# Optimization experiments

Measured on AMD Instinct MI355X. Metric: run time of the kernel, lower is better.

The kernel has to match this reference:

```python
import jax, jax.numpy as jnp
import numpy as np

N_NODES = 100000
N_REL = 8
F_IN, F_HID, F_OUT = 64, 64, 32
N_EDGES = 1000000


def rgcn_conv(x, W, root, bias, src, dst, edge_type):
    """PyG RGCNConv with default aggr='mean': out[i] = sum_r mean_{j in N_r(i)} W_r x_j + root x_i + bias."""
    R, _, O = W.shape
    N = x.shape[0]
    # Transform every node under every relation: [R, N, O]
    h = jnp.einsum('nf,rfo->rno', x, W)
    # Gather per-edge messages: [E, O]
    msg = h[edge_type, src]
    # Per-(relation, dst) mean aggregation via combined segment ids
    seg = edge_type * N + dst
    sums = jax.ops.segment_sum(msg, seg, num_segments=R * N).reshape(R, N, O)
    cnt = jax.ops.segment_sum(jnp.ones((msg.shape[0],), msg.dtype), seg,
                              num_segments=R * N).reshape(R, N, 1)
    mean = sums / jnp.maximum(cnt, 1.0)  # empty neighborhoods -> 0
    return mean.sum(axis=0) + x @ root + bias


def setup_inputs() -> dict:
    key = jax.random.key(0)
    ks = jax.random.split(key, 9)
    s = lambda fan: 1.0 / np.sqrt(fan)
    x = jax.random.normal(ks[0], (N_NODES, F_IN), jnp.float32)
    edge_index = jax.random.randint(ks[1], (2, N_EDGES), 0, N_NODES, jnp.int64)
    edge_type = jax.random.randint(ks[2], (N_EDGES,), 0, N_REL, jnp.int64)
    W1 = jax.random.normal(ks[3], (N_REL, F_IN, F_HID), jnp.float32) * s(F_IN)
    root1 = jax.random.normal(ks[4], (F_IN, F_HID), jnp.float32) * s(F_IN)
    b1 = jnp.zeros((F_HID,), jnp.float32)
    W2 = jax.random.normal(ks[5], (N_REL, F_HID, F_OUT), jnp.float32) * s(F_HID)
    root2 = jax.random.normal(ks[6], (F_HID, F_OUT), jnp.float32) * s(F_HID)
    b2 = jnp.zeros((F_OUT,), jnp.float32)
    return {"x": x, "W1": W1, "root1": root1, "b1": b1,
            "W2": W2, "root2": root2, "b2": b2,
            "edge_index": edge_index, "edge_type": edge_type}


def reference(x, W1, root1, b1, W2, root2, b2, edge_index, edge_type):
    src, dst = edge_index[0], edge_index[1]
    # encode (dropout is identity in eval mode)
    h = jax.nn.relu(rgcn_conv(x, W1, root1, b1, src, dst, edge_type))
    z = rgcn_conv(h, W2, root2, b2, src, dst, edge_type)
    # decode: gather-dot-product link scores over the same edge list
    return (z[src] * z[dst]).sum(axis=1)
```

## Files before the change

### kernel.cpp

```cpp
#include <hip/hip_runtime.h>

#define F_IN 64
#define F_HID 64
#define F_OUT 32
#define NREL 8
#define SCAP 6144
#define RCAP 10240
#define MAXBUCK 200
#define PA_PE 16

typedef __attribute__((ext_vector_type(8))) short bfrag;
typedef __attribute__((ext_vector_type(4))) float ffrag;

__device__ inline unsigned short f2bf(float f) {
  unsigned u = __float_as_uint(f);
  unsigned r = (u + 0x7fffu + ((u >> 16) & 1u)) >> 16;
  return (unsigned short)r;
}
__device__ inline unsigned bf16pair(float lo, float hi) {
  return (unsigned)f2bf(lo) | ((unsigned)f2bf(hi) << 16);
}
__device__ inline float bflo(unsigned u) { return __uint_as_float(u << 16); }
__device__ inline float bfhi(unsigned u) { return __uint_as_float(u & 0xffff0000u); }

__device__ inline void acc8(float (&acc)[8], float s, uint4 g) {
  acc[0] += s * bflo(g.x); acc[1] += s * bfhi(g.x);
  acc[2] += s * bflo(g.y); acc[3] += s * bfhi(g.y);
  acc[4] += s * bflo(g.z); acc[5] += s * bfhi(g.z);
  acc[6] += s * bflo(g.w); acc[7] += s * bfhi(g.w);
}
__device__ inline float dot8(uint4 a, uint4 b) {
  return bflo(a.x) * bflo(b.x) + bfhi(a.x) * bfhi(b.x) +
         bflo(a.y) * bflo(b.y) + bfhi(a.y) * bfhi(b.y) +
         bflo(a.z) * bflo(b.z) + bfhi(a.z) * bfhi(b.z) +
         bflo(a.w) * bflo(b.w) + bfhi(a.w) * bfhi(b.w);
}

template <int O, bool PERMK>
__device__ inline void wprep_one(int t, const float* __restrict__ W,
                                 const float* __restrict__ root,
                                 unsigned short* __restrict__ Wf) {
  constexpr int CT = O / 16;
  int l = t & 63;
  int s = (t >> 6) & 1;
  int rc = t >> 7;
  int c = rc % CT;
  int r = rc / CT;
  const float* wsrc = (r < NREL) ? W + (size_t)r * 64 * O : root;
  unsigned short* dst = Wf + (size_t)t * 8;
  int col = c * 16 + (l & 15);
  int k0 = s * 32 + ((l >> 4) * 8);
#pragma unroll
  for (int j = 0; j < 8; ++j) {
    int k = k0 + j;
    if (PERMK) k = (k & 3) * 16 + (k >> 2);
    dst[j] = f2bf(wsrc[(size_t)k * O + col]);
  }
}

__global__ __launch_bounds__(256) void prep_kernel(
    const float* __restrict__ W1, const float* __restrict__ root1,
    const float* __restrict__ W2, const float* __restrict__ root2,
    unsigned short* __restrict__ wf1, unsigned short* __restrict__ wf2,
    int* __restrict__ gcur, int nbuck) {
  int gid = blockIdx.x * 256 + threadIdx.x;
  const int J1 = (NREL + 1) * (F_HID / 16) * 2 * 64;
  const int J2 = (NREL + 1) * (F_OUT / 16) * 2 * 64;
  if (gid < J1) {
    wprep_one<F_HID, false>(gid, W1, root1, wf1);
  } else if (gid < J1 + J2) {
    wprep_one<F_OUT, true>(gid - J1, W2, root2, wf2);
  } else if (gid - J1 - J2 < nbuck) {
    int b = gid - J1 - J2;
    gcur[b] = b * SCAP;
  }
}

__device__ void binA_body(
    const int* __restrict__ src, const int* __restrict__ dst,
    const int* __restrict__ et, int* __restrict__ gcur,
    unsigned* __restrict__ staging, int E) {
  __shared__ int hist[MAXBUCK * 4];
  __shared__ int wbase[MAXBUCK * 4];
  const int tid = threadIdx.x;
  const int wave = tid >> 6;
  for (int i = tid; i < MAXBUCK * 4; i += 256) hist[i] = 0;
  __syncthreads();
  const int base = blockIdx.x * (256 * PA_PE);
  int dv[PA_PE], rk[PA_PE];
#pragma unroll
  for (int j = 0; j < PA_PE; ++j) {
    int e = base + j * 256 + tid;
    if (e < E) {
      int d = dst[e];
      dv[j] = d;
      rk[j] = atomicAdd(&hist[(d >> 9) * 4 + wave], 1);
    } else {
      dv[j] = -1;
    }
  }
  __syncthreads();
  for (int b = tid; b < MAXBUCK; b += 256) {
    int h0 = hist[b * 4 + 0], h1 = hist[b * 4 + 1];
    int h2 = hist[b * 4 + 2], h3 = hist[b * 4 + 3];
    int tot = h0 + h1 + h2 + h3;
    int gb = tot ? atomicAdd(&gcur[b], tot) : 0;
    wbase[b * 4 + 0] = gb;
    wbase[b * 4 + 1] = gb + h0;
    wbase[b * 4 + 2] = gb + h0 + h1;
    wbase[b * 4 + 3] = gb + h0 + h1 + h2;
  }
  __syncthreads();
#pragma unroll
  for (int j = 0; j < PA_PE; ++j) {
    if (dv[j] >= 0) {
      int e = base + j * 256 + tid;
      unsigned pk = (unsigned)src[e] | ((unsigned)et[e] << 17) |
                    ((unsigned)(dv[j] & 511) << 20);
      staging[wbase[(dv[j] >> 9) * 4 + wave] + rk[j]] = pk;
    }
  }
}

__global__ __launch_bounds__(256) void binB_kernel(
    const unsigned* __restrict__ staging, const int* __restrict__ gcur,
    int2* __restrict__ rec, int* __restrict__ startsA, int* __restrict__ endsA,
    int N) {
  __shared__ int cnt8[512 * 8];
  __shared__ int cur[512];
  __shared__ int tsum[256];
  const int b = blockIdx.x;
  const int tid = threadIdx.x;
  const int n0 = b << 9;
  const int nn = min(512, N - n0);
  const int cnt_b = gcur[b] - b * SCAP;
  const unsigned* st = staging + (size_t)b * SCAP;
  for (int i = tid; i < 512 * 8; i += 256) cnt8[i] = 0;
  __syncthreads();
  for (int i = tid; i < cnt_b; i += 256) {
    unsigned e = st[i];
    atomicAdd(&cnt8[((e >> 20) & 511) * 8 + ((e >> 17) & 7)], 1);
  }
  __syncthreads();
  const int na = 2 * tid, nb = 2 * tid + 1;
  int deg0 = 0, deg1 = 0;
#pragma unroll
  for (int r = 0; r < 8; ++r) {
    deg0 += cnt8[na * 8 + r];
    deg1 += cnt8[nb * 8 + r];
  }
  const int pd0 = (deg0 + 7) & ~7, pd1 = (deg1 + 7) & ~7;
  tsum[tid] = pd0 + pd1;
  __syncthreads();
  for (int off = 1; off < 256; off <<= 1) {
    int v = (tid >= off) ? tsum[tid - off] : 0;
    __syncthreads();
    tsum[tid] += v;
    __syncthreads();
  }
  const int excl = tsum[tid] - (pd0 + pd1);
  const int s0 = b * RCAP + excl;
  const int s1 = s0 + pd0;
  if (na < nn) { startsA[n0 + na] = s0; endsA[n0 + na] = s0 + pd0; cur[na] = s0; }
  if (nb < nn) { startsA[n0 + nb] = s1; endsA[n0 + nb] = s1 + pd1; cur[nb] = s1; }
  __syncthreads();
  for (int i = tid; i < 512 * 8; i += 256) {
    int cc = cnt8[i];
    ((float*)cnt8)[i] = cc > 0 ? 1.0f / (float)cc : 0.0f;
  }
  __syncthreads();
  for (int i = tid; i < cnt_b; i += 256) {
    unsigned e = st[i];
    int s = e & 0x1FFFF;
    int r = (e >> 17) & 7;
    int dl = (e >> 20) & 511;
    int pos = atomicAdd(&cur[dl], 1);
    rec[pos] = make_int2(r * N + s, ((const int*)cnt8)[dl * 8 + r]);
  }
  __syncthreads();
  if (na < nn) for (int p = cur[na]; p < s0 + pd0; ++p) rec[p] = make_int2(0, 0);
  if (nb < nn) for (int p = cur[nb]; p < s1 + pd1; ++p) rec[p] = make_int2(0, 0);
}

template <int O, bool F32IN>
__device__ void transform_body(int blk, const void* __restrict__ Xv,
                               const unsigned short* __restrict__ Wf,
                               unsigned short* __restrict__ H, int N) {
  constexpr int CT = O / 16;
  const int w = threadIdx.x >> 6;
  const int l = threadIdx.x & 63;
  const int nb = blk * 64;
  int arow = nb + w * 16 + (l & 15);
  if (arow >= N) arow = N - 1;
  bfrag a0, a1;
  if (F32IN) {
    const float* xf = (const float*)Xv + (size_t)arow * 64 + ((l >> 4) * 8);
    float4 v0 = *(const float4*)(xf);
    float4 v1 = *(const float4*)(xf + 4);
    float4 v2 = *(const float4*)(xf + 32);
    float4 v3 = *(const float4*)(xf + 36);
    a0[0] = (short)f2bf(v0.x); a0[1] = (short)f2bf(v0.y);
    a0[2] = (short)f2bf(v0.z); a0[3] = (short)f2bf(v0.w);
    a0[4] = (short)f2bf(v1.x); a0[5] = (short)f2bf(v1.y);
    a0[6] = (short)f2bf(v1.z); a0[7] = (short)f2bf(v1.w);
    a1[0] = (short)f2bf(v2.x); a1[1] = (short)f2bf(v2.y);
    a1[2] = (short)f2bf(v2.z); a1[3] = (short)f2bf(v2.w);
    a1[4] = (short)f2bf(v3.x); a1[5] = (short)f2bf(v3.y);
    a1[6] = (short)f2bf(v3.z); a1[7] = (short)f2bf(v3.w);
  } else {
    const unsigned short* xp = (const unsigned short*)Xv + (size_t)arow * 64 + ((l >> 4) * 8);
    a0 = *(const bfrag*)(xp);
    a1 = *(const bfrag*)(xp + 32);
  }
  const int rbase = nb + w * 16 + ((l >> 4) << 2);
  for (int r = 0; r < NREL + 1; ++r) {
    const unsigned short* wb = Wf + ((size_t)r * CT * 2 * 64 + l) * 8;
    ffrag acc[CT];
#pragma unroll
    for (int c = 0; c < CT; ++c) {
      bfrag b0 = *(const bfrag*)(wb + (size_t)(c * 2 + 0) * 512);
      bfrag b1 = *(const bfrag*)(wb + (size_t)(c * 2 + 1) * 512);
      ffrag z = {0.f, 0.f, 0.f, 0.f};
      acc[c] = __builtin_amdgcn_mfma_f32_16x16x32_bf16(a0, b0, z, 0, 0, 0);
      acc[c] = __builtin_amdgcn_mfma_f32_16x16x32_bf16(a1, b1, acc[c], 0, 0, 0);
    }
#pragma unroll
    for (int i = 0; i < 4; ++i) {
      int row = rbase + i;
      if (row < N) {
        if (O == 64) {
          uint2 v;
          v.x = bf16pair(acc[0][i], acc[1][i]);
          v.y = bf16pair(acc[2][i], acc[3][i]);
          *(uint2*)(H + ((size_t)r * N + row) * 64 + (l & 15) * 4) = v;
        } else {
          *(unsigned*)(H + ((size_t)r * N + row) * 32 + (l & 15) * 2) =
              bf16pair(acc[0][i], acc[1][i]);
        }
      }
    }
  }
}

__global__ __launch_bounds__(256) void binA_t1_kernel(
    const int* __restrict__ src, const int* __restrict__ dst,
    const int* __restrict__ et, int* __restrict__ gcur,
    unsigned* __restrict__ staging, int E, int nbinA,
    const float* __restrict__ x, const unsigned short* __restrict__ wf1,
    unsigned short* __restrict__ h, int N) {
  if ((int)blockIdx.x < nbinA) {
    binA_body(src, dst, et, gcur, staging, E);
  } else {
    transform_body<F_HID, true>((int)blockIdx.x - nbinA, x, wf1, h, N);
  }
}

__global__ __launch_bounds__(256) void transform2_kernel(
    const unsigned short* __restrict__ Xb, const unsigned short* __restrict__ Wf,
    unsigned short* __restrict__ H, int N) {
  transform_body<F_OUT, false>((int)blockIdx.x, Xb, Wf, H, N);
}

template <int O, bool RELU>
__global__ __launch_bounds__(256) void csr_agg_kernel(
    const unsigned* __restrict__ H, const int* __restrict__ startsA,
    const int* __restrict__ endsA, const int2* __restrict__ rec,
    const float* __restrict__ bias, unsigned* __restrict__ Y, int N) {
  constexpr int C = O / 8;
  constexpr int NPB = 256 / C;
  constexpr int HROW = O / 2;
  constexpr int CT = O / 16;
  int t = threadIdx.x;
  int n = blockIdx.x * NPB + t / C;
  int c = t % C;
  if (n >= N) return;
  float acc[8];
  uint4 rr = *(const uint4*)(H + ((size_t)(NREL * N) + n) * HROW + c * 4);
#pragma unroll
  for (int j = 0; j < 8; ++j) {
    int q = c * 8 + j;
    acc[j] = bias[(q % CT) * 16 + q / CT];
  }
  acc[0] += bflo(rr.x); acc[1] += bfhi(rr.x);
  acc[2] += bflo(rr.y); acc[3] += bfhi(rr.y);
  acc[4] += bflo(rr.z); acc[5] += bfhi(rr.z);
  acc[6] += bflo(rr.w); acc[7] += bfhi(rr.w);
  int p = startsA[n];
  int end = endsA[n];
  for (; p < end; p += 8) {
    int4 e01 = *(const int4*)(rec + p);
    int4 e23 = *(const int4*)(rec + p + 2);
    int4 e45 = *(const int4*)(rec + p + 4);
    int4 e67 = *(const int4*)(rec + p + 6);
    uint4 g0 = *(const uint4*)(H + (size_t)e01.x * HROW + c * 4);
    uint4 g1 = *(const uint4*)(H + (size_t)e01.z * HROW + c * 4);
    uint4 g2 = *(const uint4*)(H + (size_t)e23.x * HROW + c * 4);
    uint4 g3 = *(const uint4*)(H + (size_t)e23.z * HROW + c * 4);
    uint4 g4 = *(const uint4*)(H + (size_t)e45.x * HROW + c * 4);
    uint4 g5 = *(const uint4*)(H + (size_t)e45.z * HROW + c * 4);
    uint4 g6 = *(const uint4*)(H + (size_t)e67.x * HROW + c * 4);
    uint4 g7 = *(const uint4*)(H + (size_t)e67.z * HROW + c * 4);
    acc8(acc, __int_as_float(e01.y), g0);
    acc8(acc, __int_as_float(e01.w), g1);
    acc8(acc, __int_as_float(e23.y), g2);
    acc8(acc, __int_as_float(e23.w), g3);
    acc8(acc, __int_as_float(e45.y), g4);
    acc8(acc, __int_as_float(e45.w), g5);
    acc8(acc, __int_as_float(e67.y), g6);
    acc8(acc, __int_as_float(e67.w), g7);
  }
  if (RELU) {
#pragma unroll
    for (int j = 0; j < 8; ++j) acc[j] = fmaxf(acc[j], 0.f);
  }
  uint4 o;
  o.x = bf16pair(acc[0], acc[1]);
  o.y = bf16pair(acc[2], acc[3]);
  o.z = bf16pair(acc[4], acc[5]);
  o.w = bf16pair(acc[6], acc[7]);
  *(uint4*)(Y + (size_t)n * HROW + c * 4) = o;
}

__global__ __launch_bounds__(256) void decode_kernel(
    const unsigned* __restrict__ Z, const int* __restrict__ src,
    const int* __restrict__ dst, float* __restrict__ out, int E) {
  int e = blockIdx.x * blockDim.x + threadIdx.x;
  if (e >= E) return;
  const uint4* zs = (const uint4*)(Z + (size_t)src[e] * 16);
  const uint4* zd = (const uint4*)(Z + (size_t)dst[e] * 16);
  uint4 a0 = zs[0], a1 = zs[1], a2 = zs[2], a3 = zs[3];
  uint4 b0 = zd[0], b1 = zd[1], b2 = zd[2], b3 = zd[3];
  out[e] = dot8(a0, b0) + dot8(a1, b1) + dot8(a2, b2) + dot8(a3, b3);
}

extern "C" void kernel_launch(void* const* d_in, const int* in_sizes, int n_in,
                              void* d_out, int out_size, void* d_ws, size_t ws_size,
                              hipStream_t stream) {
  const float* x     = (const float*)d_in[0];
  const float* W1    = (const float*)d_in[1];
  const float* root1 = (const float*)d_in[2];
  const float* b1    = (const float*)d_in[3];
  const float* W2    = (const float*)d_in[4];
  const float* root2 = (const float*)d_in[5];
  const float* b2    = (const float*)d_in[6];
  const int*   ei    = (const int*)d_in[7];
  const int*   et    = (const int*)d_in[8];

  const int N = in_sizes[0] / F_IN;
  const int E = in_sizes[8];
  const int nbuck = (N + 511) >> 9;
  const int nbinA = (E + 256 * PA_PE - 1) / (256 * PA_PE);
  const int nT1 = (N + 63) / 64;
  const int* srcp = ei;
  const int* dstp = ei + E;

  char* ws = (char*)d_ws;
  int*            gcur    = (int*)(ws + 0);
  unsigned*       staging = (unsigned*)(ws + 4096);
  int*            startsA = (int*)(ws + 4919296);
  int*            endsA   = (int*)(ws + 5319296);
  int2*           rec     = (int2*)(ws + 5719296);
  unsigned short* wf1     = (unsigned short*)(ws + 21775616);
  unsigned short* wf2     = (unsigned short*)(ws + 21849344);
  unsigned short* h       = (unsigned short*)(ws + 21886208);
  unsigned short* hmid    = (unsigned short*)(ws + 137086208);
  unsigned short* z       = (unsigned short*)(ws + 149886208);

  prep_kernel<<<28, 256, 0, stream>>>(W1, root1, W2, root2, wf1, wf2, gcur, nbuck);

  binA_t1_kernel<<<nbinA + nT1, 256, 0, stream>>>(
      srcp, dstp, et, gcur, staging, E, nbinA, x, wf1, h, N);

  binB_kernel<<<nbuck, 256, 0, stream>>>(staging, gcur, rec, startsA, endsA, N);

  csr_agg_kernel<F_HID, true>
      <<<(N + 31) / 32, 256, 0, stream>>>((const unsigned*)h, startsA, endsA, rec,
                                          b1, (unsigned*)hmid, N);

  transform2_kernel<<<(N + 63) / 64, 256, 0, stream>>>(hmid, wf2, h, N);
  csr_agg_kernel<F_OUT, false>
      <<<(N + 63) / 64, 256, 0, stream>>>((const unsigned*)h, startsA, endsA, rec,
                                          b2, (unsigned*)z, N);

  decode_kernel<<<(E + 255) / 256, 256, 0, stream>>>((const unsigned*)z, srcp, dstp,
                                                     (float*)d_out, E);
}
```

Before: 161.2 us.

## Split transform and aggregation stages to co-schedule them with bin and aggregate kernels

Splits the first-layer transform so part of it runs alongside binA and the rest fills the small binB launch. Splits the first aggregation in two, so the second half runs in the same launch as the second-layer transform over rows the first half has already finished. Adds a separate h2 buffer so the second transform does not overwrite h1 while it is still being read. The aim is to fill idle compute units during under-occupied stages. In exchange it adds one more launch, uses more workspace, and relies on fixed split sizes (600 and 1800 blocks).

```diff
diff --git a/kernel.cpp b/kernel.cpp
--- a/kernel.cpp
+++ b/kernel.cpp
@@ -122,14 +122,13 @@
   }
 }
 
-__global__ __launch_bounds__(256) void binB_kernel(
-    const unsigned* __restrict__ staging, const int* __restrict__ gcur,
+__device__ void binB_body(
+    int b, const unsigned* __restrict__ staging, const int* __restrict__ gcur,
     int2* __restrict__ rec, int* __restrict__ startsA, int* __restrict__ endsA,
     int N) {
   __shared__ int cnt8[512 * 8];
   __shared__ int cur[512];
   __shared__ int tsum[256];
-  const int b = blockIdx.x;
   const int tid = threadIdx.x;
   const int n0 = b << 9;
   const int nn = min(512, N - n0);
@@ -242,28 +241,9 @@
   }
 }
 
-__global__ __launch_bounds__(256) void binA_t1_kernel(
-    const int* __restrict__ src, const int* __restrict__ dst,
-    const int* __restrict__ et, int* __restrict__ gcur,
-    unsigned* __restrict__ staging, int E, int nbinA,
-    const float* __restrict__ x, const unsigned short* __restrict__ wf1,
-    unsigned short* __restrict__ h, int N) {
-  if ((int)blockIdx.x < nbinA) {
-    binA_body(src, dst, et, gcur, staging, E);
-  } else {
-    transform_body<F_HID, true>((int)blockIdx.x - nbinA, x, wf1, h, N);
-  }
-}
-
-__global__ __launch_bounds__(256) void transform2_kernel(
-    const unsigned short* __restrict__ Xb, const unsigned short* __restrict__ Wf,
-    unsigned short* __restrict__ H, int N) {
-  transform_body<F_OUT, false>((int)blockIdx.x, Xb, Wf, H, N);
-}
-
 template <int O, bool RELU>
-__global__ __launch_bounds__(256) void csr_agg_kernel(
-    const unsigned* __restrict__ H, const int* __restrict__ startsA,
+__device__ void csr_agg_body(
+    int blk, const unsigned* __restrict__ H, const int* __restrict__ startsA,
     const int* __restrict__ endsA, const int2* __restrict__ rec,
     const float* __restrict__ bias, unsigned* __restrict__ Y, int N) {
   constexpr int C = O / 8;
@@ -271,7 +251,7 @@
   constexpr int HROW = O / 2;
   constexpr int CT = O / 16;
   int t = threadIdx.x;
-  int n = blockIdx.x * NPB + t / C;
+  int n = blk * NPB + t / C;
   int c = t % C;
   if (n >= N) return;
   float acc[8];
@@ -321,6 +301,67 @@
   *(uint4*)(Y + (size_t)n * HROW + c * 4) = o;
 }
 
+__global__ __launch_bounds__(256) void binA_t1a_kernel(
+    const int* __restrict__ src, const int* __restrict__ dst,
+    const int* __restrict__ et, int* __restrict__ gcur,
+    unsigned* __restrict__ staging, int E, int nbinA,
+    const float* __restrict__ x, const unsigned short* __restrict__ wf1,
+    unsigned short* __restrict__ h1, int N) {
+  if ((int)blockIdx.x < nbinA) {
+    binA_body(src, dst, et, gcur, staging, E);
+  } else {
+    transform_body<F_HID, true>((int)blockIdx.x - nbinA, x, wf1, h1, N);
+  }
+}
+
+__global__ __launch_bounds__(256) void binB_t1b_kernel(
+    const unsigned* __restrict__ staging, const int* __restrict__ gcur,
+    int2* __restrict__ rec, int* __restrict__ startsA, int* __restrict__ endsA,
+    int nbuck, int nT1a, const float* __restrict__ x,
+    const unsigned short* __restrict__ wf1, unsigned short* __restrict__ h1,
+    int N) {
+  if ((int)blockIdx.x < nbuck) {
+    binB_body((int)blockIdx.x, staging, gcur, rec, startsA, endsA, N);
+  } else {
+    transform_body<F_HID, true>(nT1a + (int)blockIdx.x - nbuck, x, wf1, h1, N);
+  }
+}
+
+__global__ __launch_bounds__(256) void agg1a_kernel(
+    const unsigned* __restrict__ H, const int* __restrict__ startsA,
+    const int* __restrict__ endsA, const int2* __restrict__ rec,
+    const float* __restrict__ bias, unsigned* __restrict__ Y, int N) {
+  csr_agg_body<F_HID, true>((int)blockIdx.x, H, startsA, endsA, rec, bias, Y, N);
+}
+
+__global__ __launch_bounds__(256) void agg1b_t2a_kernel(
+    const unsigned* __restrict__ H1, const int* __restrict__ startsA,
+    const int* __restrict__ endsA, const int2* __restrict__ rec,
+    const float* __restrict__ b1, unsigned* __restrict__ hmid,
+    int nAgg1a, int nAgg1b, const unsigned short* __restrict__ wf2,
+    unsigned short* __restrict__ h2, int N) {
+  if ((int)blockIdx.x < nAgg1b) {
+    csr_agg_body<F_HID, true>(nAgg1a + (int)blockIdx.x, H1, startsA, endsA, rec,
+                              b1, hmid, N);
+  } else {
+    transform_body<F_OUT, false>((int)blockIdx.x - nAgg1b,
+                                 (const unsigned short*)hmid, wf2, h2, N);
+  }
+}
+
+__global__ __launch_bounds__(256) void t2b_kernel(
+    const unsigned short* __restrict__ hmid, const unsigned short* __restrict__ wf2,
+    unsigned short* __restrict__ h2, int nT2a, int N) {
+  transform_body<F_OUT, false>(nT2a + (int)blockIdx.x, hmid, wf2, h2, N);
+}
+
+__global__ __launch_bounds__(256) void agg2_kernel(
+    const unsigned* __restrict__ H2, const int* __restrict__ startsA,
+    const int* __restrict__ endsA, const int2* __restrict__ rec,
+    const float* __restrict__ bias, unsigned* __restrict__ Y, int N) {
+  csr_agg_body<F_OUT, false>((int)blockIdx.x, H2, startsA, endsA, rec, bias, Y, N);
+}
+
 __global__ __launch_bounds__(256) void decode_kernel(
     const unsigned* __restrict__ Z, const int* __restrict__ src,
     const int* __restrict__ dst, float* __restrict__ out, int E) {
@@ -351,6 +392,15 @@
   const int nbuck = (N + 511) >> 9;
   const int nbinA = (E + 256 * PA_PE - 1) / (256 * PA_PE);
   const int nT1 = (N + 63) / 64;
+  const int nT1a = nT1 < 600 ? nT1 : 600;
+  const int nT1b = nT1 - nT1a;
+  const int nAgg1 = (N + 31) / 32;
+  const int nAgg1a = nAgg1 < 1800 ? nAgg1 : 1800;
+  const int nAgg1b = nAgg1 - nAgg1a;
+  const int nT2 = (N + 63) / 64;
+  int nT2a = (nAgg1a * 32) / 64;
+  if (nT2a > nT2) nT2a = nT2;
+  const int nT2b = nT2 - nT2a;
   const int* srcp = ei;
   const int* dstp = ei + E;
 
@@ -362,25 +412,30 @@
   int2*           rec     = (int2*)(ws + 5719296);
   unsigned short* wf1     = (unsigned short*)(ws + 21775616);
   unsigned short* wf2     = (unsigned short*)(ws + 21849344);
-  unsigned short* h       = (unsigned short*)(ws + 21886208);
+  unsigned short* h1      = (unsigned short*)(ws + 21886208);
   unsigned short* hmid    = (unsigned short*)(ws + 137086208);
   unsigned short* z       = (unsigned short*)(ws + 149886208);
+  unsigned short* h2      = (unsigned short*)(ws + 156286208);
 
   prep_kernel<<<28, 256, 0, stream>>>(W1, root1, W2, root2, wf1, wf2, gcur, nbuck);
 
-  binA_t1_kernel<<<nbinA + nT1, 256, 0, stream>>>(
-      srcp, dstp, et, gcur, staging, E, nbinA, x, wf1, h, N);
-
-  binB_kernel<<<nbuck, 256, 0, stream>>>(staging, gcur, rec, startsA, endsA, N);
-
-  csr_agg_kernel<F_HID, true>
-      <<<(N + 31) / 32, 256, 0, stream>>>((const unsigned*)h, startsA, endsA, rec,
-                                          b1, (unsigned*)hmid, N);
-
-  transform2_kernel<<<(N + 63) / 64, 256, 0, stream>>>(hmid, wf2, h, N);
-  csr_agg_kernel<F_OUT, false>
-      <<<(N + 63) / 64, 256, 0, stream>>>((const unsigned*)h, startsA, endsA, rec,
-                                          b2, (unsigned*)z, N);
+  binA_t1a_kernel<<<nbinA + nT1a, 256, 0, stream>>>(
+      srcp, dstp, et, gcur, staging, E, nbinA, x, wf1, h1, N);
+
+  binB_t1b_kernel<<<nbuck + nT1b, 256, 0, stream>>>(
+      staging, gcur, rec, startsA, endsA, nbuck, nT1a, x, wf1, h1, N);
+
+  agg1a_kernel<<<nAgg1a, 256, 0, stream>>>(
+      (const unsigned*)h1, startsA, endsA, rec, b1, (unsigned*)hmid, N);
+
+  agg1b_t2a_kernel<<<nAgg1b + nT2a, 256, 0, stream>>>(
+      (const unsigned*)h1, startsA, endsA, rec, b1, (unsigned*)hmid,
+      nAgg1a, nAgg1b, wf2, h2, N);
+
+  t2b_kernel<<<nT2b, 256, 0, stream>>>(hmid, wf2, h2, nT2a, N);
+
+  agg2_kernel<<<(N + 63) / 64, 256, 0, stream>>>(
+      (const unsigned*)h2, startsA, endsA, rec, b2, (unsigned*)z, N);
 
   decode_kernel<<<(E + 255) / 256, 256, 0, stream>>>((const unsigned*)z, srcp, dstp,
                                                      (float*)d_out, E);
```

Result: faster. 157.0 us (-2.6%).
